# Performance work log

Measured on AMD Instinct MI355X. Metric: run time of the kernel, lower is better.

The kernel has to match this reference:

```python
import jax, jax.numpy as jnp
import numpy as np

NEG_INF = jnp.float32(-9e15)  # matches torch's -9e15 zero_vec
ALPHA = 0.2  # LeakyReLU negative slope


def setup_inputs() -> dict:
    key = jax.random.key(0)
    k1, k2, k3, k4, k5 = jax.random.split(key, 5)
    B, N, DIN, DOUT = 8, 2048, 128, 64
    h = jax.random.normal(k1, (B, N, DIN), dtype=jnp.float32)
    adj = jax.random.randint(k2, (B, N, N), 0, 2).astype(jnp.int32)
    mask = jax.random.randint(k3, (B, N), 0, 2).astype(jnp.int32)
    # learned params: W is nn.Linear(dim_in, dim_out, bias=False) -> store as [DIN, DOUT]
    W = jax.random.normal(k4, (DIN, DOUT), dtype=jnp.float32) / np.sqrt(DIN)
    # a is [2*dim_out, 1] in torch; store flat [2*DOUT]
    a = jax.random.normal(k5, (2 * DOUT,), dtype=jnp.float32) * 0.1
    return {"h": h, "adj": adj, "mask": mask, "W": W, "a": a}


def reference(h, adj, mask, W, a):
    # h: [B,N,DIN], adj: [B,N,N] int, mask: [B,N] int, W: [DIN,DOUT], a: [2*DOUT]
    dout = W.shape[1]
    z = h @ W  # [B,N,DOUT]
    # e_ij = LeakyReLU([z_i||z_j] . a) = LeakyReLU(z_i.a1 + z_j.a2)
    a1, a2 = a[:dout], a[dout:]
    s1 = jnp.einsum("bnd,d->bn", z, a1)  # contribution of source node i
    s2 = jnp.einsum("bnd,d->bn", z, a2)  # contribution of target node j
    e = jax.nn.leaky_relu(s1[:, :, None] + s2[:, None, :], negative_slope=ALPHA)  # [B,N,N]
    att = jnp.where(adj > 0, e, NEG_INF)
    mask2d = mask[:, :, None] * mask[:, None, :]  # [B,N,N]
    att = jnp.where(mask2d > 0, att, NEG_INF)
    att = jax.nn.softmax(att, axis=-1)
    h_prime = jnp.einsum("bij,bjd->bid", att, z)  # [B,N,DOUT]
    return jax.nn.elu(h_prime)  # concat=True path
```

## Files before the change

kernel.cpp:

```cpp
#include <hip/hip_runtime.h>

#define BB 8
#define NN 2048
#define DIN 128
#define DOUT 64
#define ALPHA_NS 0.2f
#define ITILE 16
#define JTILE 64
#define NWAVE 4
#define TTOT (NN / (JTILE * NWAVE))
#define ZBLK 1024

typedef __attribute__((ext_vector_type(4))) int int4v;
typedef __attribute__((ext_vector_type(4))) short short4v;
typedef __attribute__((ext_vector_type(4))) unsigned short ushort4v;
typedef __attribute__((ext_vector_type(4))) float float4v;

__device__ __forceinline__ unsigned short f32_to_bf16_rne(float x) {
  unsigned u = __builtin_bit_cast(unsigned, x);
  u += 0x7FFFu + ((u >> 16) & 1u);
  return (unsigned short)(u >> 16);
}

__global__ __launch_bounds__(256, 4) void gat_prep(
    const float* __restrict__ h, const float* __restrict__ W,
    const float* __restrict__ a, const int* __restrict__ adj,
    const int* __restrict__ mask, unsigned* __restrict__ packedC,
    unsigned short* __restrict__ zF, float* __restrict__ s1,
    float* __restrict__ s2) {
  __shared__ float shbuf[6144];
  const int tid = threadIdx.x;
  const int w = tid >> 6, lane = tid & 63;

  if (blockIdx.x >= ZBLK) {
    const int gw = (blockIdx.x - ZBLK) * 4 + w;
    const int jg = gw & 7;
    const int iw = (gw >> 3) & 63;
    const int b = gw >> 9;
    const int j0 = jg * 256 + lane * 4;
    const int4v mv = *reinterpret_cast<const int4v*>(mask + b * NN + j0);
    const int* ap = adj + ((long)(b * NN + iw * 32)) * NN + j0;
    unsigned w0 = 0, w1 = 0, w2 = 0, w3 = 0;
#pragma unroll
    for (int r = 0; r < 32; ++r) {
      const int4v av = __builtin_nontemporal_load(
          reinterpret_cast<const int4v*>(ap + (long)r * NN));
      w0 |= ((unsigned)(av.x > 0)) << r;
      w1 |= ((unsigned)(av.y > 0)) << r;
      w2 |= ((unsigned)(av.z > 0)) << r;
      w3 |= ((unsigned)(av.w > 0)) << r;
    }
    int4v st;
    st.x = (int)(w0 & (mv.x > 0 ? ~0u : 0u));
    st.y = (int)(w1 & (mv.y > 0 ? ~0u : 0u));
    st.z = (int)(w2 & (mv.z > 0 ? ~0u : 0u));
    st.w = (int)(w3 & (mv.w > 0 ? ~0u : 0u));
    *reinterpret_cast<int4v*>(packedC + (size_t)(b * 64 + iw) * NN + j0) = st;
    return;
  }

  const int zbid = blockIdx.x;
  const long r0 = (long)zbid * 16;
  float (*hS)[DIN] = reinterpret_cast<float(*)[DIN]>(shbuf);
  float (*accW)[16][DOUT] =
      reinterpret_cast<float(*)[16][DOUT]>(shbuf + 16 * DIN);

  float Wr[32];
#pragma unroll
  for (int kk = 0; kk < 32; ++kk) Wr[kk] = W[(w * 32 + kk) * DOUT + lane];

  {
    const int r = tid >> 4, c = (tid & 15) * 8;
    const float* src = h + (r0 + r) * DIN + c;
    *reinterpret_cast<float4*>(&hS[r][c]) = *reinterpret_cast<const float4*>(src);
    *reinterpret_cast<float4*>(&hS[r][c + 4]) =
        *reinterpret_cast<const float4*>(src + 4);
  }
  __syncthreads();

#pragma unroll
  for (int r = 0; r < 16; ++r) {
    float acc = 0.f;
#pragma unroll
    for (int k4 = 0; k4 < 8; ++k4) {
      const float4 h4 = *reinterpret_cast<const float4*>(&hS[r][w * 32 + k4 * 4]);
      acc = fmaf(h4.x, Wr[k4 * 4 + 0], acc);
      acc = fmaf(h4.y, Wr[k4 * 4 + 1], acc);
      acc = fmaf(h4.z, Wr[k4 * 4 + 2], acc);
      acc = fmaf(h4.w, Wr[k4 * 4 + 3], acc);
    }
    accW[w][r][lane] = acc;
  }
  __syncthreads();

  unsigned short zt4[4];
#pragma unroll
  for (int it = 0; it < 4; ++it) {
    const int i = w * 4 + it;
    const int d = lane;
    const float zv =
        accW[0][i][d] + accW[1][i][d] + accW[2][i][d] + accW[3][i][d];
    zt4[it] = f32_to_bf16_rne(zv);
    float v1 = zv * a[d];
    float v2 = zv * a[DOUT + d];
#pragma unroll
    for (int off = 32; off; off >>= 1) {
      v1 += __shfl_xor(v1, off);
      v2 += __shfl_xor(v2, off);
    }
    if (lane == 0) {
      s1[r0 + i] = v1;
      s2[r0 + i] = v2;
    }
  }
  {
    const int b = zbid >> 7;
    const int bloc = zbid & 127;
    const int jb = bloc >> 2;
    const int ks = bloc & 3;
    const int dt = lane >> 4, row16 = lane & 15;
    ushort4v v;
    v.x = zt4[0]; v.y = zt4[1]; v.z = zt4[2]; v.w = zt4[3];
    const size_t e = ((size_t)(b * 32 + jb)) * 4096 +
                     (size_t)(((dt * 4 + ks) * 64 + w * 16 + row16) * 4);
    *reinterpret_cast<ushort4v*>(zF + e) = v;
  }
}

__global__ __launch_bounds__(256, 4) void gat_attn(
    const unsigned short* __restrict__ zF, const float* __restrict__ s1g,
    const float* __restrict__ s2g, const unsigned* __restrict__ packedC,
    const int* __restrict__ mask, float* __restrict__ out) {
  const int lid = (blockIdx.x & 7) * 128 + (blockIdx.x >> 3);
  const int b = lid >> 7;
  const int i0 = (lid & 127) * ITILE;
  const int tid = threadIdx.x;
  const int w = tid >> 6, lane = tid & 63;
  const int row16 = lane & 15, kgrp = lane >> 4;

  __shared__ __align__(16) unsigned short pA[NWAVE][ITILE][72];
  __shared__ float accS[NWAVE][ITILE][DOUT];
  __shared__ float Lred[NWAVE][ITILE];

  float s1r[ITILE];
  {
    const float v = (lane < ITILE) ? s1g[b * NN + i0 + lane] : 0.f;
#pragma unroll
    for (int i = 0; i < ITILE; ++i) s1r[i] = __shfl(v, i);
  }
  const int mvv = (lane < ITILE) ? mask[b * NN + i0 + lane] : 0;
  const unsigned mmask = (unsigned)__ballot(mvv > 0) & 0xFFFFu;

  float4v acc[5];
#pragma unroll
  for (int dt = 0; dt < 5; ++dt) acc[dt] = (float4v){0.f, 0.f, 0.f, 0.f};

  const short4v ones =
      (row16 == 0) ? short4v{(short)0x3F80, (short)0x3F80, (short)0x3F80,
                             (short)0x3F80}
                   : short4v{0, 0, 0, 0};

  const unsigned* pcb = packedC + (size_t)(b * 64 + (i0 >> 5)) * NN;
  const int ibit = i0 & 16;
  const unsigned short* ztb = zF + (size_t)(b * 32) * 4096 + lane * 4;

  unsigned aw0 = pcb[(0 * NWAVE + w) * JTILE + lane];
  unsigned aw1 = pcb[(1 * NWAVE + w) * JTILE + lane];
  float s20 = s2g[b * NN + (0 * NWAVE + w) * JTILE + lane];
  float s21 = s2g[b * NN + (1 * NWAVE + w) * JTILE + lane];
  short4v bfr[16];
  {
    const unsigned short* t0 = ztb + (size_t)w * 4096;
#pragma unroll
    for (int ks = 0; ks < 4; ++ks)
#pragma unroll
      for (int dt = 0; dt < 4; ++dt)
        bfr[ks * 4 + dt] = __builtin_bit_cast(
            short4v,
            *reinterpret_cast<const ushort4v*>(t0 + (dt * 4 + ks) * 256));
  }

#pragma unroll 1
  for (int t = 0; t < TTOT; ++t) {
    unsigned aw2 = 0;
    float s22 = 0.f;
    if (t + 2 < TTOT) {
      const int j0n = ((t + 2) * NWAVE + w) * JTILE;
      aw2 = pcb[j0n + lane];
      s22 = s2g[b * NN + j0n + lane];
    }
#pragma unroll
    for (int i = 0; i < ITILE; ++i) {
      float e = s1r[i] + s20;
      e = fmaxf(e, ALPHA_NS * e);
      float pv = ((aw0 >> (ibit + i)) & 1u) ? __expf(e) : 0.f;
      if (!((mmask >> i) & 1u)) pv = 1.0f;
      pA[w][i][lane] = f32_to_bf16_rne(pv);
    }
    const unsigned short* tn = ztb + (size_t)((t + 1) * NWAVE + w) * 4096;
    __builtin_amdgcn_s_setprio(1);
#pragma unroll
    for (int ks = 0; ks < 2; ++ks) {
      const short4v af = __builtin_bit_cast(
          short4v,
          *reinterpret_cast<const ushort4v*>(&pA[w][row16][ks * 16 + kgrp * 4]));
      acc[4] =
          __builtin_amdgcn_mfma_f32_16x16x16bf16_1k(af, ones, acc[4], 0, 0, 0);
#pragma unroll
      for (int dt = 0; dt < 4; ++dt)
        acc[dt] = __builtin_amdgcn_mfma_f32_16x16x16bf16_1k(af, bfr[ks * 4 + dt],
                                                            acc[dt], 0, 0, 0);
    }
    __builtin_amdgcn_s_setprio(0);
    if (t + 1 < TTOT) {
#pragma unroll
      for (int ks = 0; ks < 2; ++ks)
#pragma unroll
        for (int dt = 0; dt < 4; ++dt)
          bfr[ks * 4 + dt] = __builtin_bit_cast(
              short4v,
              *reinterpret_cast<const ushort4v*>(tn + (dt * 4 + ks) * 256));
    }
    __builtin_amdgcn_s_setprio(1);
#pragma unroll
    for (int ks = 2; ks < 4; ++ks) {
      const short4v af = __builtin_bit_cast(
          short4v,
          *reinterpret_cast<const ushort4v*>(&pA[w][row16][ks * 16 + kgrp * 4]));
      acc[4] =
          __builtin_amdgcn_mfma_f32_16x16x16bf16_1k(af, ones, acc[4], 0, 0, 0);
#pragma unroll
      for (int dt = 0; dt < 4; ++dt)
        acc[dt] = __builtin_amdgcn_mfma_f32_16x16x16bf16_1k(af, bfr[ks * 4 + dt],
                                                            acc[dt], 0, 0, 0);
    }
    __builtin_amdgcn_s_setprio(0);
    if (t + 1 < TTOT) {
#pragma unroll
      for (int ks = 2; ks < 4; ++ks)
#pragma unroll
        for (int dt = 0; dt < 4; ++dt)
          bfr[ks * 4 + dt] = __builtin_bit_cast(
              short4v,
              *reinterpret_cast<const ushort4v*>(tn + (dt * 4 + ks) * 256));
      aw0 = aw1; aw1 = aw2;
      s20 = s21; s21 = s22;
    }
  }

  if (row16 == 0) {
#pragma unroll
    for (int r = 0; r < 4; ++r) Lred[w][kgrp * 4 + r] = acc[4][r];
  }
#pragma unroll
  for (int dt = 0; dt < 4; ++dt) {
#pragma unroll
    for (int r = 0; r < 4; ++r)
      accS[w][kgrp * 4 + r][dt * 16 + row16] = acc[dt][r];
  }
  __syncthreads();

#pragma unroll
  for (int it = 0; it < 4; ++it) {
    const int i = (tid >> 6) + it * 4;
    const int d = tid & 63;
    const float L = Lred[0][i] + Lred[1][i] + Lred[2][i] + Lred[3][i];
    const float v = accS[0][i][d] + accS[1][i][d] + accS[2][i][d] + accS[3][i][d];
    const float hp = v / L;
    const float r = hp > 0.f ? hp : (__expf(hp) - 1.f);
    out[((long)b * NN + i0 + i) * DOUT + d] = r;
  }
}

extern "C" void kernel_launch(void* const* d_in, const int* in_sizes, int n_in,
                              void* d_out, int out_size, void* d_ws, size_t ws_size,
                              hipStream_t stream) {
  const float* h = (const float*)d_in[0];
  const int* adj = (const int*)d_in[1];
  const int* mask = (const int*)d_in[2];
  const float* W = (const float*)d_in[3];
  const float* a = (const float*)d_in[4];
  float* out = (float*)d_out;

  unsigned short* zF = (unsigned short*)d_ws;
  float* s1 = (float*)((char*)d_ws + (size_t)BB * NN * DOUT * 2);
  float* s2 = s1 + (size_t)BB * NN;
  unsigned* packedC = (unsigned*)(s2 + (size_t)BB * NN);

  gat_prep<<<dim3(ZBLK + 1024), dim3(256), 0, stream>>>(h, W, a, adj, mask,
                                                        packedC, zF, s1, s2);
  gat_attn<<<dim3(NN / ITILE * BB), dim3(256), 0, stream>>>(zF, s1, s2, packedC,
                                                            mask, out);
}
```

Baseline: 53.84 us.

## Read adjacency directly in attention kernel, drop bit-packing pass

Removes the separate adjacency bit-packing stage from the prep kernel. The attention kernel now reads int32 adjacency tiles directly, one int4 per lane, and converts probabilities with packed bf16 conversion instructions. The column mask is folded into s2 as a large negative sentinel so its exp underflows to zero. This avoids writing and re-reading the packed bitmask, but the adjacency traffic now sits inside the attention loop and its latency is hidden only by a one-step prefetch.

```diff
diff --git a/kernel.cpp b/kernel.cpp
--- a/kernel.cpp
+++ b/kernel.cpp
@@ -9,7 +9,6 @@
 #define JTILE 64
 #define NWAVE 4
 #define TTOT (NN / (JTILE * NWAVE))
-#define ZBLK 1024
 
 typedef __attribute__((ext_vector_type(4))) int int4v;
 typedef __attribute__((ext_vector_type(4))) short short4v;
@@ -22,43 +21,14 @@
   return (unsigned short)(u >> 16);
 }
 
-__global__ __launch_bounds__(256, 4) void gat_prep(
+__global__ __launch_bounds__(256, 4) void gat_zproj(
     const float* __restrict__ h, const float* __restrict__ W,
-    const float* __restrict__ a, const int* __restrict__ adj,
-    const int* __restrict__ mask, unsigned* __restrict__ packedC,
+    const float* __restrict__ a, const int* __restrict__ mask,
     unsigned short* __restrict__ zF, float* __restrict__ s1,
     float* __restrict__ s2) {
   __shared__ float shbuf[6144];
   const int tid = threadIdx.x;
   const int w = tid >> 6, lane = tid & 63;
-
-  if (blockIdx.x >= ZBLK) {
-    const int gw = (blockIdx.x - ZBLK) * 4 + w;
-    const int jg = gw & 7;
-    const int iw = (gw >> 3) & 63;
-    const int b = gw >> 9;
-    const int j0 = jg * 256 + lane * 4;
-    const int4v mv = *reinterpret_cast<const int4v*>(mask + b * NN + j0);
-    const int* ap = adj + ((long)(b * NN + iw * 32)) * NN + j0;
-    unsigned w0 = 0, w1 = 0, w2 = 0, w3 = 0;
-#pragma unroll
-    for (int r = 0; r < 32; ++r) {
-      const int4v av = __builtin_nontemporal_load(
-          reinterpret_cast<const int4v*>(ap + (long)r * NN));
-      w0 |= ((unsigned)(av.x > 0)) << r;
-      w1 |= ((unsigned)(av.y > 0)) << r;
-      w2 |= ((unsigned)(av.z > 0)) << r;
-      w3 |= ((unsigned)(av.w > 0)) << r;
-    }
-    int4v st;
-    st.x = (int)(w0 & (mv.x > 0 ? ~0u : 0u));
-    st.y = (int)(w1 & (mv.y > 0 ? ~0u : 0u));
-    st.z = (int)(w2 & (mv.z > 0 ? ~0u : 0u));
-    st.w = (int)(w3 & (mv.w > 0 ? ~0u : 0u));
-    *reinterpret_cast<int4v*>(packedC + (size_t)(b * 64 + iw) * NN + j0) = st;
-    return;
-  }
-
   const int zbid = blockIdx.x;
   const long r0 = (long)zbid * 16;
   float (*hS)[DIN] = reinterpret_cast<float(*)[DIN]>(shbuf);
@@ -110,7 +80,7 @@
     }
     if (lane == 0) {
       s1[r0 + i] = v1;
-      s2[r0 + i] = v2;
+      s2[r0 + i] = (mask[r0 + i] > 0) ? v2 : -30000.0f;
     }
   }
   {
@@ -129,7 +99,7 @@
 
 __global__ __launch_bounds__(256, 4) void gat_attn(
     const unsigned short* __restrict__ zF, const float* __restrict__ s1g,
-    const float* __restrict__ s2g, const unsigned* __restrict__ packedC,
+    const float* __restrict__ s2g, const int* __restrict__ adj,
     const int* __restrict__ mask, float* __restrict__ out) {
   const int lid = (blockIdx.x & 7) * 128 + (blockIdx.x >> 3);
   const int b = lid >> 7;
@@ -137,19 +107,20 @@
   const int tid = threadIdx.x;
   const int w = tid >> 6, lane = tid & 63;
   const int row16 = lane & 15, kgrp = lane >> 4;
+  const int rq = lane >> 4;
+  const int jq = (lane & 15) * 4;
 
   __shared__ __align__(16) unsigned short pA[NWAVE][ITILE][72];
   __shared__ float accS[NWAVE][ITILE][DOUT];
   __shared__ float Lred[NWAVE][ITILE];
 
-  float s1r[ITILE];
-  {
-    const float v = (lane < ITILE) ? s1g[b * NN + i0 + lane] : 0.f;
-#pragma unroll
-    for (int i = 0; i < ITILE; ++i) s1r[i] = __shfl(v, i);
-  }
-  const int mvv = (lane < ITILE) ? mask[b * NN + i0 + lane] : 0;
-  const unsigned mmask = (unsigned)__ballot(mvv > 0) & 0xFFFFu;
+  float s1q[4];
+  unsigned mbits = 0;
+#pragma unroll
+  for (int q = 0; q < 4; ++q) {
+    s1q[q] = s1g[b * NN + i0 + q * 4 + rq];
+    mbits |= (mask[b * NN + i0 + q * 4 + rq] > 0 ? 1u : 0u) << q;
+  }
 
   float4v acc[5];
 #pragma unroll
@@ -160,14 +131,15 @@
                              (short)0x3F80}
                    : short4v{0, 0, 0, 0};
 
-  const unsigned* pcb = packedC + (size_t)(b * 64 + (i0 >> 5)) * NN;
-  const int ibit = i0 & 16;
+  const int* abase = adj + (size_t)(b * NN + i0) * NN;
   const unsigned short* ztb = zF + (size_t)(b * 32) * 4096 + lane * 4;
 
-  unsigned aw0 = pcb[(0 * NWAVE + w) * JTILE + lane];
-  unsigned aw1 = pcb[(1 * NWAVE + w) * JTILE + lane];
-  float s20 = s2g[b * NN + (0 * NWAVE + w) * JTILE + lane];
-  float s21 = s2g[b * NN + (1 * NWAVE + w) * JTILE + lane];
+  int4v adjq[4];
+#pragma unroll
+  for (int q = 0; q < 4; ++q)
+    adjq[q] = *reinterpret_cast<const int4v*>(
+        abase + (size_t)(q * 4 + rq) * NN + w * JTILE + jq);
+  float4 s2v = *reinterpret_cast<const float4*>(s2g + b * NN + w * JTILE + jq);
   short4v bfr[16];
   {
     const unsigned short* t0 = ztb + (size_t)w * 4096;
@@ -182,20 +154,36 @@
 
 #pragma unroll 1
   for (int t = 0; t < TTOT; ++t) {
-    unsigned aw2 = 0;
-    float s22 = 0.f;
-    if (t + 2 < TTOT) {
-      const int j0n = ((t + 2) * NWAVE + w) * JTILE;
-      aw2 = pcb[j0n + lane];
-      s22 = s2g[b * NN + j0n + lane];
-    }
-#pragma unroll
-    for (int i = 0; i < ITILE; ++i) {
-      float e = s1r[i] + s20;
-      e = fmaxf(e, ALPHA_NS * e);
-      float pv = ((aw0 >> (ibit + i)) & 1u) ? __expf(e) : 0.f;
-      if (!((mmask >> i) & 1u)) pv = 1.0f;
-      pA[w][i][lane] = f32_to_bf16_rne(pv);
+#pragma unroll
+    for (int q = 0; q < 4; ++q) {
+      float sc0 = s1q[q] + s2v.x;
+      float sc1 = s1q[q] + s2v.y;
+      float sc2 = s1q[q] + s2v.z;
+      float sc3 = s1q[q] + s2v.w;
+      sc0 = fmaxf(sc0, ALPHA_NS * sc0);
+      sc1 = fmaxf(sc1, ALPHA_NS * sc1);
+      sc2 = fmaxf(sc2, ALPHA_NS * sc2);
+      sc3 = fmaxf(sc3, ALPHA_NS * sc3);
+      float p0 = (adjq[q].x > 0) ? __expf(sc0) : 0.f;
+      float p1 = (adjq[q].y > 0) ? __expf(sc1) : 0.f;
+      float p2 = (adjq[q].z > 0) ? __expf(sc2) : 0.f;
+      float p3 = (adjq[q].w > 0) ? __expf(sc3) : 0.f;
+      if (!((mbits >> q) & 1u)) {
+        p0 = p1 = p2 = p3 = 1.0f;
+      }
+      unsigned lo, hi;
+      asm("v_cvt_pk_bf16_f32 %0, %1, %2" : "=v"(lo) : "v"(p0), "v"(p1));
+      asm("v_cvt_pk_bf16_f32 %0, %1, %2" : "=v"(hi) : "v"(p2), "v"(p3));
+      uint2 pk; pk.x = lo; pk.y = hi;
+      *reinterpret_cast<uint2*>(&pA[w][q * 4 + rq][jq]) = pk;
+    }
+    if (t + 1 < TTOT) {
+      const int j0n = ((t + 1) * NWAVE + w) * JTILE;
+#pragma unroll
+      for (int q = 0; q < 4; ++q)
+        adjq[q] = *reinterpret_cast<const int4v*>(
+            abase + (size_t)(q * 4 + rq) * NN + j0n + jq);
+      s2v = *reinterpret_cast<const float4*>(s2g + b * NN + j0n + jq);
     }
     const unsigned short* tn = ztb + (size_t)((t + 1) * NWAVE + w) * 4096;
     __builtin_amdgcn_s_setprio(1);
@@ -243,8 +231,6 @@
           bfr[ks * 4 + dt] = __builtin_bit_cast(
               short4v,
               *reinterpret_cast<const ushort4v*>(tn + (dt * 4 + ks) * 256));
-      aw0 = aw1; aw1 = aw2;
-      s20 = s21; s21 = s22;
     }
   }
 
@@ -285,10 +271,8 @@
   unsigned short* zF = (unsigned short*)d_ws;
   float* s1 = (float*)((char*)d_ws + (size_t)BB * NN * DOUT * 2);
   float* s2 = s1 + (size_t)BB * NN;
-  unsigned* packedC = (unsigned*)(s2 + (size_t)BB * NN);
-
-  gat_prep<<<dim3(ZBLK + 1024), dim3(256), 0, stream>>>(h, W, a, adj, mask,
-                                                        packedC, zF, s1, s2);
-  gat_attn<<<dim3(NN / ITILE * BB), dim3(256), 0, stream>>>(zF, s1, s2, packedC,
+
+  gat_zproj<<<dim3(1024), dim3(256), 0, stream>>>(h, W, a, mask, zF, s1, s2);
+  gat_attn<<<dim3(NN / ITILE * BB), dim3(256), 0, stream>>>(zF, s1, s2, adj,
                                                             mask, out);
 }
```

Result: faster. 43.19 us, median of 3 (-19.8%).
